# Performance work log

Measured on AMD Instinct MI355X. Metric: run time of the kernel, lower is better.

## Reference

```python
import jax, jax.numpy as jnp
import numpy as np

N = 50000
E = 800000
D_IN = 128
D_OUT = 128


def setup_inputs() -> dict:
    key = jax.random.key(0)
    ks = jax.random.split(key, 12)
    x = jax.random.normal(ks[0], (N, D_IN), dtype=jnp.float32)
    edge_index = jax.random.randint(ks[1], (2, E), 0, N, dtype=jnp.int64)
    importance = jax.random.uniform(ks[2], (N, 1), dtype=jnp.float32)
    s = 1.0 / np.sqrt(D_IN)
    W_msg = jax.random.uniform(ks[3], (D_IN, D_OUT), jnp.float32, -s, s)
    b_msg = jax.random.uniform(ks[4], (D_OUT,), jnp.float32, -s, s)
    s2 = 1.0 / np.sqrt(D_IN + D_OUT)
    W_upd = jax.random.uniform(ks[5], (D_IN + D_OUT, D_OUT), jnp.float32, -s2, s2)
    b_upd = jax.random.uniform(ks[6], (D_OUT,), jnp.float32, -s2, s2)
    s3 = 1.0 / np.sqrt(D_OUT + 1)
    W_gate = jax.random.uniform(ks[7], (D_OUT + 1, D_OUT), jnp.float32, -s3, s3)
    b_gate = jax.random.uniform(ks[8], (D_OUT,), jnp.float32, -s3, s3)
    s4 = 1.0 / np.sqrt(D_OUT)
    W_imp = jax.random.uniform(ks[9], (D_OUT, 1), jnp.float32, -s4, s4)
    b_imp = jax.random.uniform(ks[10], (1,), jnp.float32, -s4, s4)
    return {
        "x": x, "edge_index": edge_index, "importance": importance,
        "W_msg": W_msg, "b_msg": b_msg, "W_upd": W_upd, "b_upd": b_upd,
        "W_gate": W_gate, "b_gate": b_gate, "W_imp": W_imp, "b_imp": b_imp,
    }


def reference(x, edge_index, importance, W_msg, b_msg, W_upd, b_upd,
              W_gate, b_gate, W_imp, b_imp):
    src, dst = edge_index[0], edge_index[1]
    # message: lin_message(x_j). Transform nodes once (N < E), then gather.
    m_nodes = x @ W_msg + b_msg              # [N, D_OUT]
    msgs = m_nodes[src]                      # [E, D_OUT] gather
    aggr = jax.ops.segment_sum(msgs, dst, num_segments=N)  # [N, D_OUT] scatter-add
    # update: lin_update(cat([x, aggr]))
    conv_out = jnp.concatenate([x, aggr], axis=-1) @ W_upd + b_upd  # [N, D_OUT]
    # sigmoid-gated residual mix with importance
    gate_in = jnp.concatenate([conv_out, importance], axis=-1)      # [N, D_OUT+1]
    gate = jax.nn.sigmoid(gate_in @ W_gate + b_gate)
    out = gate * conv_out + (1.0 - gate) * x
    propagated_importance = out @ W_imp + b_imp                     # [N, 1]
    return out, propagated_importance
```

## Files before the change

### kernel.cpp

```cpp
#include <hip/hip_runtime.h>
#include <hip/hip_bf16.h>

#define D 128

#define PW 132
#define PX 129

__global__ void count_deg(const int* __restrict__ ei, int* __restrict__ deg, int E) {
    int e = blockIdx.x * 256 + threadIdx.x;
    if (e < E) atomicAdd(&deg[ei[E + e]], 1);
}

__global__ __launch_bounds__(256) void scan_kernel(const int* __restrict__ deg,
                                                   int* __restrict__ rowstart,
                                                   int* __restrict__ cursor, int n) {
    __shared__ int tsum[257];
    int tid = threadIdx.x;
    int chunk = (n + 255) / 256;
    int lo = tid * chunk;
    int hi = lo + chunk; if (hi > n) hi = n;
    int s = 0;
    for (int i = lo; i < hi; ++i) s += deg[i];
    tsum[tid] = s;
    __syncthreads();
    if (tid == 0) {
        int run = 0;
        for (int i = 0; i < 256; ++i) { int t = tsum[i]; tsum[i] = run; run += t; }
        tsum[256] = run;
    }
    __syncthreads();
    int run = tsum[tid];
    for (int i = lo; i < hi; ++i) {
        rowstart[i] = run; cursor[i] = run; run += deg[i];
    }
    if (tid == 0) rowstart[n] = tsum[256];
}

__global__ void fill_csr(const int* __restrict__ ei, int* __restrict__ cursor,
                         int* __restrict__ csr, int E) {
    int e = blockIdx.x * 256 + threadIdx.x;
    if (e < E) {
        int s = ei[e];
        int d = ei[E + e];
        int p = atomicAdd(&cursor[d], 1);
        csr[p] = s;
    }
}

__global__ __launch_bounds__(256, 1) void gemm_msg(const float* __restrict__ x,
                                                   const float* __restrict__ W,
                                                   const float* __restrict__ b,
                                                   float* __restrict__ out, int n) {
    __shared__ __align__(16) float Ws[D * PW];
    __shared__ __align__(16) float Ts[D * PX];
    const int tid = threadIdx.x;
    const int R0 = blockIdx.x * 128;

    for (int t = 0; t < 64; ++t) {
        int e = t * 256 + tid;
        int r = e >> 7, c = e & 127;
        Ws[r * PW + c] = W[e];
        int gr = R0 + r; if (gr >= n) gr = n - 1;
        Ts[c * PX + r] = x[(long)gr * D + c];
    }
    __syncthreads();

    const int tr = tid >> 4, tc = tid & 15;
    const int r0 = tr * 8, c0 = tc * 8;
    float acc[8][8];
#pragma unroll
    for (int i = 0; i < 8; ++i)
#pragma unroll
        for (int j = 0; j < 8; ++j) acc[i][j] = 0.f;

    for (int k = 0; k < D; ++k) {
        float4 wa = *(const float4*)&Ws[k * PW + c0];
        float4 wb = *(const float4*)&Ws[k * PW + c0 + 4];
        float xs[8];
#pragma unroll
        for (int i = 0; i < 8; ++i) xs[i] = Ts[k * PX + r0 + i];
#pragma unroll
        for (int i = 0; i < 8; ++i) {
            acc[i][0] += xs[i] * wa.x; acc[i][1] += xs[i] * wa.y;
            acc[i][2] += xs[i] * wa.z; acc[i][3] += xs[i] * wa.w;
            acc[i][4] += xs[i] * wb.x; acc[i][5] += xs[i] * wb.y;
            acc[i][6] += xs[i] * wb.z; acc[i][7] += xs[i] * wb.w;
        }
    }

    float bj[8];
#pragma unroll
    for (int j = 0; j < 8; ++j) bj[j] = b[c0 + j];
#pragma unroll
    for (int i = 0; i < 8; ++i) {
        int row = R0 + r0 + i;
        if (row < n) {
            float4 o0, o1;
            o0.x = acc[i][0] + bj[0]; o0.y = acc[i][1] + bj[1];
            o0.z = acc[i][2] + bj[2]; o0.w = acc[i][3] + bj[3];
            o1.x = acc[i][4] + bj[4]; o1.y = acc[i][5] + bj[5];
            o1.z = acc[i][6] + bj[6]; o1.w = acc[i][7] + bj[7];
            *(float4*)&out[(long)row * D + c0] = o0;
            *(float4*)&out[(long)row * D + c0 + 4] = o1;
        }
    }
}

__global__ __launch_bounds__(256) void aggr_kernel(const float* __restrict__ mn,
                                                   const int* __restrict__ rowstart,
                                                   const int* __restrict__ csr,
                                                   float* __restrict__ aggr, int n) {
    int gw = (blockIdx.x * 256 + threadIdx.x) >> 6;
    int lane = threadIdx.x & 63;
    if (gw >= n) return;
    int rs = rowstart[gw], re = rowstart[gw + 1];
    float ax = 0.f, ay = 0.f, bx = 0.f, by = 0.f;
    int i = rs;
    for (; i + 1 < re; i += 2) {
        int s0 = csr[i], s1 = csr[i + 1];
        float2 v0 = *(const float2*)&mn[(long)s0 * D + lane * 2];
        float2 v1 = *(const float2*)&mn[(long)s1 * D + lane * 2];
        ax += v0.x; ay += v0.y; bx += v1.x; by += v1.y;
    }
    if (i < re) {
        int s0 = csr[i];
        float2 v0 = *(const float2*)&mn[(long)s0 * D + lane * 2];
        ax += v0.x; ay += v0.y;
    }
    float2 o; o.x = ax + bx; o.y = ay + by;
    *(float2*)&aggr[(long)gw * D + lane * 2] = o;
}

__global__ __launch_bounds__(256, 1) void fused_update(
        const float* __restrict__ x, const float* __restrict__ aggr,
        const float* __restrict__ imp,
        const float* __restrict__ W_upd, const float* __restrict__ b_upd,
        const float* __restrict__ W_gate, const float* __restrict__ b_gate,
        const float* __restrict__ W_imp, const float* __restrict__ b_imp,
        float* __restrict__ out, int n) {
    __shared__ __align__(16) float Ws[D * PW];
    __shared__ __align__(16) float Ts[D * PX];
    const int tid = threadIdx.x;
    const int R0 = blockIdx.x * 128;
    const int tr = tid >> 4, tc = tid & 15;
    const int r0 = tr * 8, c0 = tc * 8;

    float acc[8][8];
#pragma unroll
    for (int i = 0; i < 8; ++i)
#pragma unroll
        for (int j = 0; j < 8; ++j) acc[i][j] = 0.f;

    for (int t = 0; t < 64; ++t) {
        int e = t * 256 + tid;
        int r = e >> 7, c = e & 127;
        Ws[r * PW + c] = W_upd[e];
        int gr = R0 + r; if (gr >= n) gr = n - 1;
        Ts[c * PX + r] = x[(long)gr * D + c];
    }
    __syncthreads();
    for (int k = 0; k < D; ++k) {
        float4 wa = *(const float4*)&Ws[k * PW + c0];
        float4 wb = *(const float4*)&Ws[k * PW + c0 + 4];
        float xs[8];
#pragma unroll
        for (int i = 0; i < 8; ++i) xs[i] = Ts[k * PX + r0 + i];
#pragma unroll
        for (int i = 0; i < 8; ++i) {
            acc[i][0] += xs[i] * wa.x; acc[i][1] += xs[i] * wa.y;
            acc[i][2] += xs[i] * wa.z; acc[i][3] += xs[i] * wa.w;
            acc[i][4] += xs[i] * wb.x; acc[i][5] += xs[i] * wb.y;
            acc[i][6] += xs[i] * wb.z; acc[i][7] += xs[i] * wb.w;
        }
    }
    __syncthreads();

    for (int t = 0; t < 64; ++t) {
        int e = t * 256 + tid;
        int r = e >> 7, c = e & 127;
        Ws[r * PW + c] = W_upd[128 * D + e];
        int gr = R0 + r; if (gr >= n) gr = n - 1;
        Ts[c * PX + r] = aggr[(long)gr * D + c];
    }
    __syncthreads();
    for (int k = 0; k < D; ++k) {
        float4 wa = *(const float4*)&Ws[k * PW + c0];
        float4 wb = *(const float4*)&Ws[k * PW + c0 + 4];
        float xs[8];
#pragma unroll
        for (int i = 0; i < 8; ++i) xs[i] = Ts[k * PX + r0 + i];
#pragma unroll
        for (int i = 0; i < 8; ++i) {
            acc[i][0] += xs[i] * wa.x; acc[i][1] += xs[i] * wa.y;
            acc[i][2] += xs[i] * wa.z; acc[i][3] += xs[i] * wa.w;
            acc[i][4] += xs[i] * wb.x; acc[i][5] += xs[i] * wb.y;
            acc[i][6] += xs[i] * wb.z; acc[i][7] += xs[i] * wb.w;
        }
    }
    __syncthreads();

#pragma unroll
    for (int j = 0; j < 8; ++j) {
        float bj = b_upd[c0 + j];
#pragma unroll
        for (int i = 0; i < 8; ++i) acc[i][j] += bj;
    }
#pragma unroll
    for (int i = 0; i < 8; ++i)
#pragma unroll
        for (int j = 0; j < 8; ++j)
            Ts[(c0 + j) * PX + r0 + i] = acc[i][j];
    for (int t = 0; t < 64; ++t) {
        int e = t * 256 + tid;
        int r = e >> 7, c = e & 127;
        Ws[r * PW + c] = W_gate[e];
    }
    __syncthreads();

    float g[8][8];
#pragma unroll
    for (int i = 0; i < 8; ++i)
#pragma unroll
        for (int j = 0; j < 8; ++j) g[i][j] = 0.f;
    for (int k = 0; k < D; ++k) {
        float4 wa = *(const float4*)&Ws[k * PW + c0];
        float4 wb = *(const float4*)&Ws[k * PW + c0 + 4];
        float xs[8];
#pragma unroll
        for (int i = 0; i < 8; ++i) xs[i] = Ts[k * PX + r0 + i];
#pragma unroll
        for (int i = 0; i < 8; ++i) {
            g[i][0] += xs[i] * wa.x; g[i][1] += xs[i] * wa.y;
            g[i][2] += xs[i] * wa.z; g[i][3] += xs[i] * wa.w;
            g[i][4] += xs[i] * wb.x; g[i][5] += xs[i] * wb.y;
            g[i][6] += xs[i] * wb.z; g[i][7] += xs[i] * wb.w;
        }
    }

    float wgl[8], bg[8], wim[8];
#pragma unroll
    for (int j = 0; j < 8; ++j) {
        wgl[j] = W_gate[128 * D + c0 + j];
        bg[j]  = b_gate[c0 + j];
        wim[j] = W_imp[c0 + j];
    }
    const float bi = b_imp[0];

#pragma unroll
    for (int i = 0; i < 8; ++i) {
        int row = R0 + r0 + i;
        int crow = row < n ? row : n - 1;
        float iv = imp[crow];
        float4 xv0 = *(const float4*)&x[(long)crow * D + c0];
        float4 xv1 = *(const float4*)&x[(long)crow * D + c0 + 4];
        float xr[8] = {xv0.x, xv0.y, xv0.z, xv0.w, xv1.x, xv1.y, xv1.z, xv1.w};
#pragma unroll
        for (int j = 0; j < 8; ++j) {
            float z = g[i][j] + iv * wgl[j] + bg[j];
            float s = 1.0f / (1.0f + expf(-z));
            g[i][j] = s * acc[i][j] + (1.0f - s) * xr[j];
        }
        if (row < n) {
            float4 o0, o1;
            o0.x = g[i][0]; o0.y = g[i][1]; o0.z = g[i][2]; o0.w = g[i][3];
            o1.x = g[i][4]; o1.y = g[i][5]; o1.z = g[i][6]; o1.w = g[i][7];
            *(float4*)&out[(long)row * D + c0] = o0;
            *(float4*)&out[(long)row * D + c0 + 4] = o1;
        }
    }

#pragma unroll
    for (int i = 0; i < 8; ++i) {
        float pi = 0.f;
#pragma unroll
        for (int j = 0; j < 8; ++j) pi += g[i][j] * wim[j];
#pragma unroll
        for (int m = 8; m >= 1; m >>= 1) pi += __shfl_xor(pi, m, 16);
        int row = R0 + r0 + i;
        if (tc == 0 && row < n) out[(long)n * D + row] = pi + bi;
    }
}

extern "C" void kernel_launch(void* const* d_in, const int* in_sizes, int n_in,
                              void* d_out, int out_size, void* d_ws, size_t ws_size,
                              hipStream_t stream) {
    const float* x      = (const float*)d_in[0];
    const int*   ei     = (const int*)d_in[1];
    const float* imp    = (const float*)d_in[2];
    const float* W_msg  = (const float*)d_in[3];
    const float* b_msg  = (const float*)d_in[4];
    const float* W_upd  = (const float*)d_in[5];
    const float* b_upd  = (const float*)d_in[6];
    const float* W_gate = (const float*)d_in[7];
    const float* b_gate = (const float*)d_in[8];
    const float* W_imp  = (const float*)d_in[9];
    const float* b_imp  = (const float*)d_in[10];
    float* out = (float*)d_out;

    const int N = in_sizes[0] / D;
    const int E = in_sizes[1] / 2;

    char* ws = (char*)d_ws;
    float* m_nodes  = (float*)ws;  ws += (size_t)N * D * sizeof(float);
    float* aggr     = (float*)ws;  ws += (size_t)N * D * sizeof(float);
    int*   deg      = (int*)ws;    ws += (size_t)N * sizeof(int);
    int*   rowstart = (int*)ws;    ws += (size_t)(N + 1) * sizeof(int);
    int*   cursor   = (int*)ws;    ws += (size_t)N * sizeof(int);
    int*   csr      = (int*)ws;    ws += (size_t)E * sizeof(int);

    hipMemsetAsync(deg, 0, (size_t)N * sizeof(int), stream);

    count_deg<<<(E + 255) / 256, 256, 0, stream>>>(ei, deg, E);
    scan_kernel<<<1, 256, 0, stream>>>(deg, rowstart, cursor, N);
    fill_csr<<<(E + 255) / 256, 256, 0, stream>>>(ei, cursor, csr, E);

    const int nblk = (N + 127) / 128;
    gemm_msg<<<nblk, 256, 0, stream>>>(x, W_msg, b_msg, m_nodes, N);

    aggr_kernel<<<((size_t)N * 64 + 255) / 256, 256, 0, stream>>>(
        m_nodes, rowstart, csr, aggr, N);

    fused_update<<<nblk, 256, 0, stream>>>(x, aggr, imp, W_upd, b_upd,
                                           W_gate, b_gate, W_imp, b_imp,
                                           out, N);
}
```

Baseline: 545.7 us.

## Shrink GEMM tiles to 64 rows with K-chunked shared memory for higher occupancy

Both dense kernels (message GEMM and fused update/gate) now work on 64-row blocks, with each thread computing 8x4 outputs instead of 8x8. The K dimension is staged through shared memory in 64-wide chunks, which cuts LDS use to about 50KB so that three blocks fit per CU (launch bounds raised to 3). With 128-row blocks there were only about 391 blocks for 256 CUs, so this doubles the block count for better load balance and latency hiding. The cost is more barriers, reloading W per block and chunk, and lower register-level reuse per thread.

```diff
diff --git a/kernel.cpp b/kernel.cpp
--- a/kernel.cpp
+++ b/kernel.cpp
@@ -2,9 +2,9 @@
 #include <hip/hip_bf16.h>
 
 #define D 128
-
-#define PW 132
-#define PX 129
+#define BR 64
+#define PWS 132
+#define PXS 65
 
 __global__ void count_deg(const int* __restrict__ ei, int* __restrict__ deg, int E) {
     int e = blockIdx.x * 256 + threadIdx.x;
@@ -47,61 +47,60 @@
     }
 }
 
-__global__ __launch_bounds__(256, 1) void gemm_msg(const float* __restrict__ x,
+__global__ __launch_bounds__(256, 3) void gemm_msg(const float* __restrict__ x,
                                                    const float* __restrict__ W,
                                                    const float* __restrict__ b,
                                                    float* __restrict__ out, int n) {
-    __shared__ __align__(16) float Ws[D * PW];
-    __shared__ __align__(16) float Ts[D * PX];
+    __shared__ __align__(16) float Ws[64 * PWS];
+    __shared__ __align__(16) float Xs[BR * PXS];
     const int tid = threadIdx.x;
-    const int R0 = blockIdx.x * 128;
-
-    for (int t = 0; t < 64; ++t) {
-        int e = t * 256 + tid;
-        int r = e >> 7, c = e & 127;
-        Ws[r * PW + c] = W[e];
-        int gr = R0 + r; if (gr >= n) gr = n - 1;
-        Ts[c * PX + r] = x[(long)gr * D + c];
-    }
-    __syncthreads();
-
-    const int tr = tid >> 4, tc = tid & 15;
-    const int r0 = tr * 8, c0 = tc * 8;
-    float acc[8][8];
+    const int R0 = blockIdx.x * BR;
+    const int tr = tid >> 5, tc = tid & 31;
+    const int r0 = tr * 8, c0 = tc * 4;
+
+    float acc[8][4];
 #pragma unroll
     for (int i = 0; i < 8; ++i)
 #pragma unroll
-        for (int j = 0; j < 8; ++j) acc[i][j] = 0.f;
-
-    for (int k = 0; k < D; ++k) {
-        float4 wa = *(const float4*)&Ws[k * PW + c0];
-        float4 wb = *(const float4*)&Ws[k * PW + c0 + 4];
-        float xs[8];
-#pragma unroll
-        for (int i = 0; i < 8; ++i) xs[i] = Ts[k * PX + r0 + i];
-#pragma unroll
-        for (int i = 0; i < 8; ++i) {
-            acc[i][0] += xs[i] * wa.x; acc[i][1] += xs[i] * wa.y;
-            acc[i][2] += xs[i] * wa.z; acc[i][3] += xs[i] * wa.w;
-            acc[i][4] += xs[i] * wb.x; acc[i][5] += xs[i] * wb.y;
-            acc[i][6] += xs[i] * wb.z; acc[i][7] += xs[i] * wb.w;
-        }
-    }
-
-    float bj[8];
-#pragma unroll
-    for (int j = 0; j < 8; ++j) bj[j] = b[c0 + j];
+        for (int j = 0; j < 4; ++j) acc[i][j] = 0.f;
+
+    for (int ch = 0; ch < 2; ++ch) {
+        const int k0 = ch * 64;
+        if (ch) __syncthreads();
+        for (int t = 0; t < 32; ++t) {
+            int e = t * 256 + tid;
+            int k = e >> 7, c = e & 127;
+            Ws[k * PWS + c] = W[(k0 + k) * D + c];
+        }
+        for (int t = 0; t < 16; ++t) {
+            int e = t * 256 + tid;
+            int r = e >> 6, c = e & 63;
+            int gr = R0 + r; if (gr >= n) gr = n - 1;
+            Xs[r * PXS + c] = x[(long)gr * D + k0 + c];
+        }
+        __syncthreads();
+        for (int k = 0; k < 64; ++k) {
+            float4 wa = *(const float4*)&Ws[k * PWS + c0];
+            float xs[8];
+#pragma unroll
+            for (int i = 0; i < 8; ++i) xs[i] = Xs[(r0 + i) * PXS + k];
+#pragma unroll
+            for (int i = 0; i < 8; ++i) {
+                acc[i][0] += xs[i] * wa.x; acc[i][1] += xs[i] * wa.y;
+                acc[i][2] += xs[i] * wa.z; acc[i][3] += xs[i] * wa.w;
+            }
+        }
+    }
+
+    const float4 bj = *(const float4*)&b[c0];
 #pragma unroll
     for (int i = 0; i < 8; ++i) {
         int row = R0 + r0 + i;
         if (row < n) {
-            float4 o0, o1;
-            o0.x = acc[i][0] + bj[0]; o0.y = acc[i][1] + bj[1];
-            o0.z = acc[i][2] + bj[2]; o0.w = acc[i][3] + bj[3];
-            o1.x = acc[i][4] + bj[4]; o1.y = acc[i][5] + bj[5];
-            o1.z = acc[i][6] + bj[6]; o1.w = acc[i][7] + bj[7];
-            *(float4*)&out[(long)row * D + c0] = o0;
-            *(float4*)&out[(long)row * D + c0 + 4] = o1;
+            float4 o;
+            o.x = acc[i][0] + bj.x; o.y = acc[i][1] + bj.y;
+            o.z = acc[i][2] + bj.z; o.w = acc[i][3] + bj.w;
+            *(float4*)&out[(long)row * D + c0] = o;
         }
     }
 }
@@ -131,119 +130,103 @@
     *(float2*)&aggr[(long)gw * D + lane * 2] = o;
 }
 
-__global__ __launch_bounds__(256, 1) void fused_update(
+__global__ __launch_bounds__(256, 3) void fused_update(
         const float* __restrict__ x, const float* __restrict__ aggr,
         const float* __restrict__ imp,
         const float* __restrict__ W_upd, const float* __restrict__ b_upd,
         const float* __restrict__ W_gate, const float* __restrict__ b_gate,
         const float* __restrict__ W_imp, const float* __restrict__ b_imp,
         float* __restrict__ out, int n) {
-    __shared__ __align__(16) float Ws[D * PW];
-    __shared__ __align__(16) float Ts[D * PX];
+    __shared__ __align__(16) float Ws[64 * PWS];
+    __shared__ __align__(16) float Xs[BR * PXS];
     const int tid = threadIdx.x;
-    const int R0 = blockIdx.x * 128;
-    const int tr = tid >> 4, tc = tid & 15;
-    const int r0 = tr * 8, c0 = tc * 8;
-
-    float acc[8][8];
+    const int R0 = blockIdx.x * BR;
+    const int tr = tid >> 5, tc = tid & 31;
+    const int r0 = tr * 8, c0 = tc * 4;
+
+    float acc[8][4];
 #pragma unroll
     for (int i = 0; i < 8; ++i)
 #pragma unroll
-        for (int j = 0; j < 8; ++j) acc[i][j] = 0.f;
-
-    for (int t = 0; t < 64; ++t) {
-        int e = t * 256 + tid;
-        int r = e >> 7, c = e & 127;
-        Ws[r * PW + c] = W_upd[e];
-        int gr = R0 + r; if (gr >= n) gr = n - 1;
-        Ts[c * PX + r] = x[(long)gr * D + c];
-    }
-    __syncthreads();
-    for (int k = 0; k < D; ++k) {
-        float4 wa = *(const float4*)&Ws[k * PW + c0];
-        float4 wb = *(const float4*)&Ws[k * PW + c0 + 4];
-        float xs[8];
-#pragma unroll
-        for (int i = 0; i < 8; ++i) xs[i] = Ts[k * PX + r0 + i];
+        for (int j = 0; j < 4; ++j) acc[i][j] = 0.f;
+
+    for (int ch = 0; ch < 4; ++ch) {
+        const int k0 = ch * 64;
+        const float* src = (ch < 2) ? x : aggr;
+        const int koff = (ch & 1) * 64;
+        if (ch) __syncthreads();
+        for (int t = 0; t < 32; ++t) {
+            int e = t * 256 + tid;
+            int k = e >> 7, c = e & 127;
+            Ws[k * PWS + c] = W_upd[(k0 + k) * D + c];
+        }
+        for (int t = 0; t < 16; ++t) {
+            int e = t * 256 + tid;
+            int r = e >> 6, c = e & 63;
+            int gr = R0 + r; if (gr >= n) gr = n - 1;
+            Xs[r * PXS + c] = src[(long)gr * D + koff + c];
+        }
+        __syncthreads();
+        for (int k = 0; k < 64; ++k) {
+            float4 wa = *(const float4*)&Ws[k * PWS + c0];
+            float xs[8];
+#pragma unroll
+            for (int i = 0; i < 8; ++i) xs[i] = Xs[(r0 + i) * PXS + k];
+#pragma unroll
+            for (int i = 0; i < 8; ++i) {
+                acc[i][0] += xs[i] * wa.x; acc[i][1] += xs[i] * wa.y;
+                acc[i][2] += xs[i] * wa.z; acc[i][3] += xs[i] * wa.w;
+            }
+        }
+    }
+
+    {
+        const float4 bu = *(const float4*)&b_upd[c0];
 #pragma unroll
         for (int i = 0; i < 8; ++i) {
-            acc[i][0] += xs[i] * wa.x; acc[i][1] += xs[i] * wa.y;
-            acc[i][2] += xs[i] * wa.z; acc[i][3] += xs[i] * wa.w;
-            acc[i][4] += xs[i] * wb.x; acc[i][5] += xs[i] * wb.y;
-            acc[i][6] += xs[i] * wb.z; acc[i][7] += xs[i] * wb.w;
-        }
-    }
-    __syncthreads();
-
-    for (int t = 0; t < 64; ++t) {
-        int e = t * 256 + tid;
-        int r = e >> 7, c = e & 127;
-        Ws[r * PW + c] = W_upd[128 * D + e];
-        int gr = R0 + r; if (gr >= n) gr = n - 1;
-        Ts[c * PX + r] = aggr[(long)gr * D + c];
-    }
-    __syncthreads();
-    for (int k = 0; k < D; ++k) {
-        float4 wa = *(const float4*)&Ws[k * PW + c0];
-        float4 wb = *(const float4*)&Ws[k * PW + c0 + 4];
-        float xs[8];
-#pragma unroll
-        for (int i = 0; i < 8; ++i) xs[i] = Ts[k * PX + r0 + i];
-#pragma unroll
-        for (int i = 0; i < 8; ++i) {
-            acc[i][0] += xs[i] * wa.x; acc[i][1] += xs[i] * wa.y;
-            acc[i][2] += xs[i] * wa.z; acc[i][3] += xs[i] * wa.w;
-            acc[i][4] += xs[i] * wb.x; acc[i][5] += xs[i] * wb.y;
-            acc[i][6] += xs[i] * wb.z; acc[i][7] += xs[i] * wb.w;
-        }
-    }
-    __syncthreads();
-
-#pragma unroll
-    for (int j = 0; j < 8; ++j) {
-        float bj = b_upd[c0 + j];
-#pragma unroll
-        for (int i = 0; i < 8; ++i) acc[i][j] += bj;
-    }
+            acc[i][0] += bu.x; acc[i][1] += bu.y;
+            acc[i][2] += bu.z; acc[i][3] += bu.w;
+        }
+    }
+
+    float g[8][4];
 #pragma unroll
     for (int i = 0; i < 8; ++i)
 #pragma unroll
-        for (int j = 0; j < 8; ++j)
-            Ts[(c0 + j) * PX + r0 + i] = acc[i][j];
-    for (int t = 0; t < 64; ++t) {
-        int e = t * 256 + tid;
-        int r = e >> 7, c = e & 127;
-        Ws[r * PW + c] = W_gate[e];
-    }
-    __syncthreads();
-
-    float g[8][8];
-#pragma unroll
-    for (int i = 0; i < 8; ++i)
-#pragma unroll
-        for (int j = 0; j < 8; ++j) g[i][j] = 0.f;
-    for (int k = 0; k < D; ++k) {
-        float4 wa = *(const float4*)&Ws[k * PW + c0];
-        float4 wb = *(const float4*)&Ws[k * PW + c0 + 4];
-        float xs[8];
-#pragma unroll
-        for (int i = 0; i < 8; ++i) xs[i] = Ts[k * PX + r0 + i];
-#pragma unroll
-        for (int i = 0; i < 8; ++i) {
-            g[i][0] += xs[i] * wa.x; g[i][1] += xs[i] * wa.y;
-            g[i][2] += xs[i] * wa.z; g[i][3] += xs[i] * wa.w;
-            g[i][4] += xs[i] * wb.x; g[i][5] += xs[i] * wb.y;
-            g[i][6] += xs[i] * wb.z; g[i][7] += xs[i] * wb.w;
-        }
-    }
-
-    float wgl[8], bg[8], wim[8];
-#pragma unroll
-    for (int j = 0; j < 8; ++j) {
-        wgl[j] = W_gate[128 * D + c0 + j];
-        bg[j]  = b_gate[c0 + j];
-        wim[j] = W_imp[c0 + j];
-    }
+        for (int j = 0; j < 4; ++j) g[i][j] = 0.f;
+
+    for (int gc = 0; gc < 2; ++gc) {
+        __syncthreads();
+        for (int t = 0; t < 32; ++t) {
+            int e = t * 256 + tid;
+            int k = e >> 7, c = e & 127;
+            Ws[k * PWS + c] = W_gate[(gc * 64 + k) * D + c];
+        }
+        if ((c0 >> 6) == gc) {
+            const int cb = c0 & 63;
+#pragma unroll
+            for (int i = 0; i < 8; ++i)
+#pragma unroll
+                for (int j = 0; j < 4; ++j)
+                    Xs[(r0 + i) * PXS + cb + j] = acc[i][j];
+        }
+        __syncthreads();
+        for (int k = 0; k < 64; ++k) {
+            float4 wa = *(const float4*)&Ws[k * PWS + c0];
+            float xs[8];
+#pragma unroll
+            for (int i = 0; i < 8; ++i) xs[i] = Xs[(r0 + i) * PXS + k];
+#pragma unroll
+            for (int i = 0; i < 8; ++i) {
+                g[i][0] += xs[i] * wa.x; g[i][1] += xs[i] * wa.y;
+                g[i][2] += xs[i] * wa.z; g[i][3] += xs[i] * wa.w;
+            }
+        }
+    }
+
+    const float4 wgl = *(const float4*)&W_gate[128 * D + c0];
+    const float4 bg  = *(const float4*)&b_gate[c0];
+    const float4 wim = *(const float4*)&W_imp[c0];
     const float bi = b_imp[0];
 
 #pragma unroll
@@ -251,31 +234,30 @@
         int row = R0 + r0 + i;
         int crow = row < n ? row : n - 1;
         float iv = imp[crow];
-        float4 xv0 = *(const float4*)&x[(long)crow * D + c0];
-        float4 xv1 = *(const float4*)&x[(long)crow * D + c0 + 4];
-        float xr[8] = {xv0.x, xv0.y, xv0.z, xv0.w, xv1.x, xv1.y, xv1.z, xv1.w};
-#pragma unroll
-        for (int j = 0; j < 8; ++j) {
-            float z = g[i][j] + iv * wgl[j] + bg[j];
-            float s = 1.0f / (1.0f + expf(-z));
-            g[i][j] = s * acc[i][j] + (1.0f - s) * xr[j];
-        }
+        float4 xv = *(const float4*)&x[(long)crow * D + c0];
+        float z0 = g[i][0] + iv * wgl.x + bg.x;
+        float z1 = g[i][1] + iv * wgl.y + bg.y;
+        float z2 = g[i][2] + iv * wgl.z + bg.z;
+        float z3 = g[i][3] + iv * wgl.w + bg.w;
+        float s0 = 1.0f / (1.0f + expf(-z0));
+        float s1 = 1.0f / (1.0f + expf(-z1));
+        float s2 = 1.0f / (1.0f + expf(-z2));
+        float s3 = 1.0f / (1.0f + expf(-z3));
+        g[i][0] = s0 * acc[i][0] + (1.0f - s0) * xv.x;
+        g[i][1] = s1 * acc[i][1] + (1.0f - s1) * xv.y;
+        g[i][2] = s2 * acc[i][2] + (1.0f - s2) * xv.z;
+        g[i][3] = s3 * acc[i][3] + (1.0f - s3) * xv.w;
         if (row < n) {
-            float4 o0, o1;
-            o0.x = g[i][0]; o0.y = g[i][1]; o0.z = g[i][2]; o0.w = g[i][3];
-            o1.x = g[i][4]; o1.y = g[i][5]; o1.z = g[i][6]; o1.w = g[i][7];
-            *(float4*)&out[(long)row * D + c0] = o0;
-            *(float4*)&out[(long)row * D + c0 + 4] = o1;
+            float4 o; o.x = g[i][0]; o.y = g[i][1]; o.z = g[i][2]; o.w = g[i][3];
+            *(float4*)&out[(long)row * D + c0] = o;
         }
     }
 
 #pragma unroll
     for (int i = 0; i < 8; ++i) {
-        float pi = 0.f;
-#pragma unroll
-        for (int j = 0; j < 8; ++j) pi += g[i][j] * wim[j];
-#pragma unroll
-        for (int m = 8; m >= 1; m >>= 1) pi += __shfl_xor(pi, m, 16);
+        float pi = g[i][0] * wim.x + g[i][1] * wim.y + g[i][2] * wim.z + g[i][3] * wim.w;
+#pragma unroll
+        for (int m = 16; m >= 1; m >>= 1) pi += __shfl_xor(pi, m, 32);
         int row = R0 + r0 + i;
         if (tc == 0 && row < n) out[(long)n * D + row] = pi + bi;
     }
@@ -314,7 +296,7 @@
     scan_kernel<<<1, 256, 0, stream>>>(deg, rowstart, cursor, N);
     fill_csr<<<(E + 255) / 256, 256, 0, stream>>>(ei, cursor, csr, E);
 
-    const int nblk = (N + 127) / 128;
+    const int nblk = (N + BR - 1) / BR;
     gemm_msg<<<nblk, 256, 0, stream>>>(x, W_msg, b_msg, m_nodes, N);
 
     aggr_kernel<<<((size_t)N * 64 + 255) / 256, 256, 0, stream>>>(
```

New measurement: 649.7 us. 1.19x slower.
